# Kernel optimization log

Measured on AMD Instinct MI355X. Metric: run time of the kernel, lower is better.

## Reference

```python
import jax, jax.numpy as jnp
import numpy as np

N_ENTITY, N_REL, DIM, H = 500000, 32, 64, 2
N_ITEM, N_MEM, BATCH, HIST = 10000, 32, 4096, 50


def setup_inputs() -> dict:
    key = jax.random.key(0)
    ks = jax.random.split(key, 10)
    return {
        "entity_emb": jax.random.normal(ks[0], (N_ENTITY, DIM), jnp.float32) * 0.05,
        "relation_emb": jax.random.normal(ks[1], (N_REL, DIM), jnp.float32) * 0.05,
        "W_w": jax.random.normal(ks[2], (1, 3 * DIM), jnp.float32) * 0.05,
        "W_b": jnp.zeros((1,), jnp.float32),
        "item_ids": jax.random.randint(ks[3], (N_ITEM,), 0, N_ENTITY, jnp.int32),
        "heads": jax.random.randint(ks[4], (H, N_ITEM, N_MEM), 0, N_ENTITY, jnp.int32),
        "relations": jax.random.randint(ks[5], (H, N_ITEM, N_MEM), 0, N_REL, jnp.int32),
        "tails": jax.random.randint(ks[6], (H, N_ITEM, N_MEM), 0, N_ENTITY, jnp.int32),
        "records_idx": jax.random.randint(ks[7], (BATCH, HIST), 0, N_ITEM, jnp.int32),
        "items": jax.random.randint(ks[8], (BATCH,), 0, N_ENTITY, jnp.int32),
    }


def reference(entity_emb, relation_emb, W_w, W_b, item_ids, heads, relations, tails, records_idx, items):
    d = entity_emb.shape[1]
    # Split the Linear(3d->1) weight so we never materialize the [n_item,m,3d] concat.
    w_h, w_r, w_t = W_w[0, :d], W_w[0, d:2 * d], W_w[0, 2 * d:]
    # Hop-0 item embedding (base entity embedding of each candidate item).
    acc = entity_emb[item_ids]  # [n_item, d]
    for h in range(heads.shape[0]):
        te = entity_emb[tails[h]]  # [n_item, m, d]
        logits = (entity_emb[heads[h]] @ w_h
                  + relation_emb[relations[h]] @ w_r
                  + te @ w_t + W_b[0])  # [n_item, m]
        # Original: sigmoid then softmax over the memory axis.
        pi = jax.nn.softmax(jax.nn.sigmoid(logits), axis=1)[..., None]
        acc = acc + (pi * te).sum(axis=1)
    # User embedding = sum of (hop-enhanced) item embeddings over history records.
    user_emb = acc[records_idx].sum(axis=1)  # [B, d]
    pair_item = entity_emb[items]            # [B, d] (raw entity embedding)
    return jax.nn.sigmoid(jnp.sum(user_emb * pair_item, axis=-1))
```

## Files before the change

kernel.cpp:

```cpp
#include <hip/hip_runtime.h>
#include <math.h>

#define DIM      64
#define N_MEM    32
#define N_ENTITY 500000
#define N_REL    32
#define N_ITEM   10000
#define HOPS     2
#define BATCH    4096
#define HIST     50

typedef float4 f4;

__global__ __launch_bounds__(256) void ripple_rdot(
    const float* __restrict__ relation_emb,
    const float* __restrict__ W_w,
    float* __restrict__ rdot)
{
    const int wave = (blockIdx.x * blockDim.x + threadIdx.x) >> 6;
    const int lane = threadIdx.x & 63;
    const int g = lane >> 4;
    const int p = lane & 15;
    const int r = wave * 4 + g;
    if (r >= N_REL) return;
    const f4 wr = ((const f4*)W_w)[16 + p];
    const f4 r4 = ((const f4*)relation_emb)[(size_t)r * 16 + p];
    float vr = r4.x * wr.x + r4.y * wr.y + r4.z * wr.z + r4.w * wr.w;
    vr += __shfl_xor(vr, 1, 64);
    vr += __shfl_xor(vr, 2, 64);
    vr += __shfl_xor(vr, 4, 64);
    vr += __shfl_xor(vr, 8, 64);
    if (p == 0) rdot[r] = vr;
}

__global__ __launch_bounds__(256) void ripple_stage1(
    const float* __restrict__ W_w,
    const float* __restrict__ W_b,
    const int*   __restrict__ heads,
    const int*   __restrict__ relations,
    const int*   __restrict__ tails,
    const float* __restrict__ entity_emb,
    const float* __restrict__ rdot,
    float*       __restrict__ accp)
{
    const int wave = (blockIdx.x * blockDim.x + threadIdx.x) >> 6;
    const int lane = threadIdx.x & 63;
    if (wave >= HOPS * N_ITEM) return;
    const int h = wave < N_ITEM ? 0 : 1;
    const int i = wave - h * N_ITEM;
    const int g = lane >> 4;
    const int p = lane & 15;

    const f4* __restrict__ E4 = (const f4*)entity_emb;
    const f4* __restrict__ W4 = (const f4*)W_w;

    const f4 wh = W4[p];
    const f4 wt = W4[32 + p];
    const float bias = W_b[0];

    const int base = wave * N_MEM + g;

    int hi[8], ri[8], ti[8];
#pragma unroll
    for (int k = 0; k < 8; ++k) {
        hi[k] = heads[base + 4 * k];
        ri[k] = relations[base + 4 * k];
        ti[k] = tails[base + 4 * k];
    }

    f4 he[8], te[8];
#pragma unroll
    for (int k = 0; k < 8; ++k) he[k] = E4[(size_t)hi[k] * 16 + p];
#pragma unroll
    for (int k = 0; k < 8; ++k) te[k] = E4[(size_t)ti[k] * 16 + p];

    float lr[8];
#pragma unroll
    for (int k = 0; k < 8; ++k) lr[k] = rdot[ri[k]];

    float part[8];
#pragma unroll
    for (int k = 0; k < 8; ++k) {
        part[k] = he[k].x * wh.x + he[k].y * wh.y + he[k].z * wh.z + he[k].w * wh.w
                + te[k].x * wt.x + te[k].y * wt.y + te[k].z * wt.z + te[k].w * wt.w;
    }

    float e[8];
    float se = 0.f;
#pragma unroll
    for (int k = 0; k < 8; ++k) {
        float v = part[k];
        v += __shfl_xor(v, 1, 64);
        v += __shfl_xor(v, 2, 64);
        v += __shfl_xor(v, 4, 64);
        v += __shfl_xor(v, 8, 64);
        const float logit = v + lr[k] + bias;
        const float sig   = 1.f / (1.f + __expf(-logit));
        const float ex    = __expf(sig);
        e[k] = ex;
        se += ex;
    }
    se += __shfl_xor(se, 16, 64);
    se += __shfl_xor(se, 32, 64);
    const float inv = 1.f / se;

    f4 acc = {0.f, 0.f, 0.f, 0.f};
#pragma unroll
    for (int k = 0; k < 8; ++k) {
        const float w = e[k] * inv;
        acc.x += w * te[k].x;
        acc.y += w * te[k].y;
        acc.z += w * te[k].z;
        acc.w += w * te[k].w;
    }

    acc.x += __shfl_xor(acc.x, 16, 64);
    acc.x += __shfl_xor(acc.x, 32, 64);
    acc.y += __shfl_xor(acc.y, 16, 64);
    acc.y += __shfl_xor(acc.y, 32, 64);
    acc.z += __shfl_xor(acc.z, 16, 64);
    acc.z += __shfl_xor(acc.z, 32, 64);
    acc.w += __shfl_xor(acc.w, 16, 64);
    acc.w += __shfl_xor(acc.w, 32, 64);
    if (g == 0) ((f4*)accp)[((size_t)i * 2 + h) * 16 + p] = acc;
}

__global__ __launch_bounds__(256) void ripple_fold(
    const float* __restrict__ entity_emb,
    const int*   __restrict__ item_ids,
    const float* __restrict__ accp,
    float*       __restrict__ folded)
{
    const int t = blockIdx.x * blockDim.x + threadIdx.x;
    if (t >= N_ITEM * 16) return;
    const int i = t >> 4;
    const int p = t & 15;
    const f4* __restrict__ E4 = (const f4*)entity_emb;
    const f4* __restrict__ A4 = (const f4*)accp;
    const f4 a  = A4[(size_t)i * 32 + p];
    const f4 b  = A4[(size_t)i * 32 + 16 + p];
    const f4 it = E4[(size_t)item_ids[i] * 16 + p];
    f4 r;
    r.x = it.x + a.x + b.x;
    r.y = it.y + a.y + b.y;
    r.z = it.z + a.z + b.z;
    r.w = it.w + a.w + b.w;
    ((f4*)folded)[(size_t)i * 16 + p] = r;
}

__global__ __launch_bounds__(256) void ripple_stage2(
    const float* __restrict__ entity_emb,
    const int*   __restrict__ records_idx,
    const int*   __restrict__ items,
    const float* __restrict__ folded,
    float*       __restrict__ out)
{
    const int wave = (blockIdx.x * blockDim.x + threadIdx.x) >> 6;
    const int lane = threadIdx.x & 63;
    if (wave >= BATCH) return;
    const int b = wave;
    const int g = lane >> 4;
    const int p = lane & 15;

    const f4* __restrict__ A4 = (const f4*)folded;
    const f4* __restrict__ E4 = (const f4*)entity_emb;

    const int rb = b * HIST;
    int idx[13];
    float wgt[13];
#pragma unroll
    for (int k = 0; k < 13; ++k) {
        const int j  = 4 * k + g;
        const int jc = j < HIST ? j : (HIST - 1);
        wgt[k] = j < HIST ? 1.f : 0.f;
        idx[k] = records_idx[rb + jc];
    }

    f4 user = {0.f, 0.f, 0.f, 0.f};
#pragma unroll
    for (int k = 0; k < 13; ++k) {
        const f4 r = A4[(size_t)idx[k] * 16 + p];
        user.x += wgt[k] * r.x;
        user.y += wgt[k] * r.y;
        user.z += wgt[k] * r.z;
        user.w += wgt[k] * r.w;
    }
    user.x += __shfl_xor(user.x, 16, 64);
    user.x += __shfl_xor(user.x, 32, 64);
    user.y += __shfl_xor(user.y, 16, 64);
    user.y += __shfl_xor(user.y, 32, 64);
    user.z += __shfl_xor(user.z, 16, 64);
    user.z += __shfl_xor(user.z, 32, 64);
    user.w += __shfl_xor(user.w, 16, 64);
    user.w += __shfl_xor(user.w, 32, 64);

    const f4 pair = E4[(size_t)items[b] * 16 + p];
    float dot = user.x * pair.x + user.y * pair.y + user.z * pair.z + user.w * pair.w;
    dot += __shfl_xor(dot, 1, 64);
    dot += __shfl_xor(dot, 2, 64);
    dot += __shfl_xor(dot, 4, 64);
    dot += __shfl_xor(dot, 8, 64);
    if (lane == 0) out[b] = 1.f / (1.f + __expf(-dot));
}

extern "C" void kernel_launch(void* const* d_in, const int* in_sizes, int n_in,
                              void* d_out, int out_size, void* d_ws, size_t ws_size,
                              hipStream_t stream) {
    const float* entity_emb   = (const float*)d_in[0];
    const float* relation_emb = (const float*)d_in[1];
    const float* W_w          = (const float*)d_in[2];
    const float* W_b          = (const float*)d_in[3];
    const int*   item_ids     = (const int*)d_in[4];
    const int*   heads        = (const int*)d_in[5];
    const int*   relations    = (const int*)d_in[6];
    const int*   tails        = (const int*)d_in[7];
    const int*   records_idx  = (const int*)d_in[8];
    const int*   items        = (const int*)d_in[9];
    float* out = (float*)d_out;

    float* rdot   = (float*)d_ws;
    float* accp   = rdot + N_REL;
    float* folded = accp + (size_t)N_ITEM * HOPS * DIM;

    ripple_rdot<<<2, 256, 0, stream>>>(relation_emb, W_w, rdot);

    const int waves1  = HOPS * N_ITEM;
    const int blocks1 = (waves1 + 3) / 4;
    ripple_stage1<<<blocks1, 256, 0, stream>>>(W_w, W_b, heads, relations, tails,
                                               entity_emb, rdot, accp);

    const int blocksF = (N_ITEM * 16 + 255) / 256;
    ripple_fold<<<blocksF, 256, 0, stream>>>(entity_emb, item_ids, accp, folded);

    const int blocks2 = (BATCH + 3) / 4;
    ripple_stage2<<<blocks2, 256, 0, stream>>>(entity_emb, records_idx, items,
                                               folded, out);
}
```

Measured before the change: 228.3 us.

## Precompute per-entity head-weight dot products to replace head embedding gathers

Adds a pass that computes the dot product of every entity row with the head slice of the linear weight, alongside the relation dots. Stage1 then gathers a single float per head index instead of a full 64-float head embedding row and its dot product. This removes the random 256-byte head-row gathers from stage1. In exchange it streams the whole entity table once per call and writes a 500k-float workspace array, most of which is never used.

```diff
diff --git a/kernel.cpp b/kernel.cpp
--- a/kernel.cpp
+++ b/kernel.cpp
@@ -12,25 +12,39 @@
 
 typedef float4 f4;
 
-__global__ __launch_bounds__(256) void ripple_rdot(
+__global__ __launch_bounds__(256) void ripple_dots(
+    const float* __restrict__ entity_emb,
     const float* __restrict__ relation_emb,
     const float* __restrict__ W_w,
+    float* __restrict__ hdot,
     float* __restrict__ rdot)
 {
     const int wave = (blockIdx.x * blockDim.x + threadIdx.x) >> 6;
     const int lane = threadIdx.x & 63;
     const int g = lane >> 4;
     const int p = lane & 15;
-    const int r = wave * 4 + g;
-    if (r >= N_REL) return;
-    const f4 wr = ((const f4*)W_w)[16 + p];
-    const f4 r4 = ((const f4*)relation_emb)[(size_t)r * 16 + p];
-    float vr = r4.x * wr.x + r4.y * wr.y + r4.z * wr.z + r4.w * wr.w;
-    vr += __shfl_xor(vr, 1, 64);
-    vr += __shfl_xor(vr, 2, 64);
-    vr += __shfl_xor(vr, 4, 64);
-    vr += __shfl_xor(vr, 8, 64);
-    if (p == 0) rdot[r] = vr;
+    const int row = wave * 4 + g;
+    if (row >= N_ENTITY + N_REL) return;
+
+    const f4* __restrict__ W4 = (const f4*)W_w;
+    float v;
+    if (row < N_ENTITY) {
+        const f4 w = W4[p];
+        const f4 e = ((const f4*)entity_emb)[(size_t)row * 16 + p];
+        v = e.x * w.x + e.y * w.y + e.z * w.z + e.w * w.w;
+    } else {
+        const f4 w = W4[16 + p];
+        const f4 e = ((const f4*)relation_emb)[(size_t)(row - N_ENTITY) * 16 + p];
+        v = e.x * w.x + e.y * w.y + e.z * w.z + e.w * w.w;
+    }
+    v += __shfl_xor(v, 1, 64);
+    v += __shfl_xor(v, 2, 64);
+    v += __shfl_xor(v, 4, 64);
+    v += __shfl_xor(v, 8, 64);
+    if (p == 0) {
+        if (row < N_ENTITY) hdot[row] = v;
+        else                rdot[row - N_ENTITY] = v;
+    }
 }
 
 __global__ __launch_bounds__(256) void ripple_stage1(
@@ -40,6 +54,7 @@
     const int*   __restrict__ relations,
     const int*   __restrict__ tails,
     const float* __restrict__ entity_emb,
+    const float* __restrict__ hdot,
     const float* __restrict__ rdot,
     float*       __restrict__ accp)
 {
@@ -54,7 +69,6 @@
     const f4* __restrict__ E4 = (const f4*)entity_emb;
     const f4* __restrict__ W4 = (const f4*)W_w;
 
-    const f4 wh = W4[p];
     const f4 wt = W4[32 + p];
     const float bias = W_b[0];
 
@@ -68,21 +82,20 @@
         ti[k] = tails[base + 4 * k];
     }
 
-    f4 he[8], te[8];
-#pragma unroll
-    for (int k = 0; k < 8; ++k) he[k] = E4[(size_t)hi[k] * 16 + p];
+    f4 te[8];
 #pragma unroll
     for (int k = 0; k < 8; ++k) te[k] = E4[(size_t)ti[k] * 16 + p];
 
-    float lr[8];
+    float lh[8], lr[8];
+#pragma unroll
+    for (int k = 0; k < 8; ++k) lh[k] = hdot[hi[k]];
 #pragma unroll
     for (int k = 0; k < 8; ++k) lr[k] = rdot[ri[k]];
 
     float part[8];
 #pragma unroll
     for (int k = 0; k < 8; ++k) {
-        part[k] = he[k].x * wh.x + he[k].y * wh.y + he[k].z * wh.z + he[k].w * wh.w
-                + te[k].x * wt.x + te[k].y * wt.y + te[k].z * wt.z + te[k].w * wt.w;
+        part[k] = te[k].x * wt.x + te[k].y * wt.y + te[k].z * wt.z + te[k].w * wt.w;
     }
 
     float e[8];
@@ -94,7 +107,7 @@
         v += __shfl_xor(v, 2, 64);
         v += __shfl_xor(v, 4, 64);
         v += __shfl_xor(v, 8, 64);
-        const float logit = v + lr[k] + bias;
+        const float logit = v + lh[k] + lr[k] + bias;
         const float sig   = 1.f / (1.f + __expf(-logit));
         const float ex    = __expf(sig);
         e[k] = ex;
@@ -219,15 +232,18 @@
     float* out = (float*)d_out;
 
     float* rdot   = (float*)d_ws;
-    float* accp   = rdot + N_REL;
+    float* hdot   = rdot + N_REL;
+    float* accp   = hdot + N_ENTITY;
     float* folded = accp + (size_t)N_ITEM * HOPS * DIM;
 
-    ripple_rdot<<<2, 256, 0, stream>>>(relation_emb, W_w, rdot);
+    const int rowsD   = N_ENTITY + N_REL;
+    const int blocksD = (rowsD + 15) / 16;
+    ripple_dots<<<blocksD, 256, 0, stream>>>(entity_emb, relation_emb, W_w, hdot, rdot);
 
     const int waves1  = HOPS * N_ITEM;
     const int blocks1 = (waves1 + 3) / 4;
     ripple_stage1<<<blocks1, 256, 0, stream>>>(W_w, W_b, heads, relations, tails,
-                                               entity_emb, rdot, accp);
+                                               entity_emb, hdot, rdot, accp);
 
     const int blocksF = (N_ITEM * 16 + 255) / 256;
     ripple_fold<<<blocksF, 256, 0, stream>>>(entity_emb, item_ids, accp, folded);
```

Measured after the change: 235.2 us. +3.0%, slower.

## Fuse both hops and fold into one stage1 wave; shuffle-broadcast indices

Applied to the files above, without the earlier changes.

Stage1 now assigns one wave per item that processes both hops and adds the base item embedding, which removes the separate fold kernel and the accp intermediate buffer. Head, relation and tail indices, plus the relation dot, are loaded once per lane with coalesced reads and broadcast with __shfl, replacing the strided per-group loads. Stage2 likewise loads the history indices once per lane and broadcasts them. In exchange the grid has half as many waves with more serial work per wave and higher register pressure, which reduces the memory-latency parallelism available for the random gathers.

```diff
diff --git a/kernel.cpp b/kernel.cpp
--- a/kernel.cpp
+++ b/kernel.cpp
@@ -41,111 +41,99 @@
     const int*   __restrict__ tails,
     const float* __restrict__ entity_emb,
     const float* __restrict__ rdot,
-    float*       __restrict__ accp)
+    const int*   __restrict__ item_ids,
+    float*       __restrict__ folded)
 {
     const int wave = (blockIdx.x * blockDim.x + threadIdx.x) >> 6;
     const int lane = threadIdx.x & 63;
-    if (wave >= HOPS * N_ITEM) return;
-    const int h = wave < N_ITEM ? 0 : 1;
-    const int i = wave - h * N_ITEM;
+    if (wave >= N_ITEM) return;
+    const int i = wave;
     const int g = lane >> 4;
     const int p = lane & 15;
 
     const f4* __restrict__ E4 = (const f4*)entity_emb;
     const f4* __restrict__ W4 = (const f4*)W_w;
-
     const f4 wh = W4[p];
     const f4 wt = W4[32 + p];
     const float bias = W_b[0];
 
-    const int base = wave * N_MEM + g;
-
-    int hi[8], ri[8], ti[8];
-#pragma unroll
-    for (int k = 0; k < 8; ++k) {
-        hi[k] = heads[base + 4 * k];
-        ri[k] = relations[base + 4 * k];
-        ti[k] = tails[base + 4 * k];
+    const int m    = lane & 31;
+    const int hsel = lane >> 5;
+    const size_t idxoff = (size_t)hsel * ((size_t)N_ITEM * N_MEM)
+                        + (size_t)i * N_MEM + m;
+    const int   hidx = heads[idxoff];
+    const int   ridx = relations[idxoff];
+    const int   tidx = tails[idxoff];
+    const float lrl  = rdot[ridx];
+
+    const f4 item = E4[(size_t)item_ids[i] * 16 + p];
+
+    f4 accs[2];
+#pragma unroll
+    for (int h = 0; h < 2; ++h) {
+        int hi[8], ti[8]; float lrv[8];
+#pragma unroll
+        for (int k = 0; k < 8; ++k) {
+            const int src = h * 32 + 4 * k + g;
+            hi[k]  = __shfl(hidx, src, 64);
+            ti[k]  = __shfl(tidx, src, 64);
+            lrv[k] = __shfl(lrl,  src, 64);
+        }
+
+        f4 he[8], te[8];
+#pragma unroll
+        for (int k = 0; k < 8; ++k) he[k] = E4[(size_t)hi[k] * 16 + p];
+#pragma unroll
+        for (int k = 0; k < 8; ++k) te[k] = E4[(size_t)ti[k] * 16 + p];
+
+        float e[8];
+        float se = 0.f;
+#pragma unroll
+        for (int k = 0; k < 8; ++k) {
+            float v = he[k].x * wh.x + he[k].y * wh.y + he[k].z * wh.z + he[k].w * wh.w
+                    + te[k].x * wt.x + te[k].y * wt.y + te[k].z * wt.z + te[k].w * wt.w;
+            v += __shfl_xor(v, 1, 64);
+            v += __shfl_xor(v, 2, 64);
+            v += __shfl_xor(v, 4, 64);
+            v += __shfl_xor(v, 8, 64);
+            const float logit = v + lrv[k] + bias;
+            const float sig   = 1.f / (1.f + __expf(-logit));
+            const float ex    = __expf(sig);
+            e[k] = ex;
+            se += ex;
+        }
+        se += __shfl_xor(se, 16, 64);
+        se += __shfl_xor(se, 32, 64);
+        const float inv = 1.f / se;
+
+        f4 acc = {0.f, 0.f, 0.f, 0.f};
+#pragma unroll
+        for (int k = 0; k < 8; ++k) {
+            const float w = e[k] * inv;
+            acc.x += w * te[k].x;
+            acc.y += w * te[k].y;
+            acc.z += w * te[k].z;
+            acc.w += w * te[k].w;
+        }
+        acc.x += __shfl_xor(acc.x, 16, 64);
+        acc.x += __shfl_xor(acc.x, 32, 64);
+        acc.y += __shfl_xor(acc.y, 16, 64);
+        acc.y += __shfl_xor(acc.y, 32, 64);
+        acc.z += __shfl_xor(acc.z, 16, 64);
+        acc.z += __shfl_xor(acc.z, 32, 64);
+        acc.w += __shfl_xor(acc.w, 16, 64);
+        acc.w += __shfl_xor(acc.w, 32, 64);
+        accs[h] = acc;
     }
 
-    f4 he[8], te[8];
-#pragma unroll
-    for (int k = 0; k < 8; ++k) he[k] = E4[(size_t)hi[k] * 16 + p];
-#pragma unroll
-    for (int k = 0; k < 8; ++k) te[k] = E4[(size_t)ti[k] * 16 + p];
-
-    float lr[8];
-#pragma unroll
-    for (int k = 0; k < 8; ++k) lr[k] = rdot[ri[k]];
-
-    float part[8];
-#pragma unroll
-    for (int k = 0; k < 8; ++k) {
-        part[k] = he[k].x * wh.x + he[k].y * wh.y + he[k].z * wh.z + he[k].w * wh.w
-                + te[k].x * wt.x + te[k].y * wt.y + te[k].z * wt.z + te[k].w * wt.w;
+    if (g == 0) {
+        f4 r;
+        r.x = item.x + accs[0].x + accs[1].x;
+        r.y = item.y + accs[0].y + accs[1].y;
+        r.z = item.z + accs[0].z + accs[1].z;
+        r.w = item.w + accs[0].w + accs[1].w;
+        ((f4*)folded)[(size_t)i * 16 + p] = r;
     }
-
-    float e[8];
-    float se = 0.f;
-#pragma unroll
-    for (int k = 0; k < 8; ++k) {
-        float v = part[k];
-        v += __shfl_xor(v, 1, 64);
-        v += __shfl_xor(v, 2, 64);
-        v += __shfl_xor(v, 4, 64);
-        v += __shfl_xor(v, 8, 64);
-        const float logit = v + lr[k] + bias;
-        const float sig   = 1.f / (1.f + __expf(-logit));
-        const float ex    = __expf(sig);
-        e[k] = ex;
-        se += ex;
-    }
-    se += __shfl_xor(se, 16, 64);
-    se += __shfl_xor(se, 32, 64);
-    const float inv = 1.f / se;
-
-    f4 acc = {0.f, 0.f, 0.f, 0.f};
-#pragma unroll
-    for (int k = 0; k < 8; ++k) {
-        const float w = e[k] * inv;
-        acc.x += w * te[k].x;
-        acc.y += w * te[k].y;
-        acc.z += w * te[k].z;
-        acc.w += w * te[k].w;
-    }
-
-    acc.x += __shfl_xor(acc.x, 16, 64);
-    acc.x += __shfl_xor(acc.x, 32, 64);
-    acc.y += __shfl_xor(acc.y, 16, 64);
-    acc.y += __shfl_xor(acc.y, 32, 64);
-    acc.z += __shfl_xor(acc.z, 16, 64);
-    acc.z += __shfl_xor(acc.z, 32, 64);
-    acc.w += __shfl_xor(acc.w, 16, 64);
-    acc.w += __shfl_xor(acc.w, 32, 64);
-    if (g == 0) ((f4*)accp)[((size_t)i * 2 + h) * 16 + p] = acc;
-}
-
-__global__ __launch_bounds__(256) void ripple_fold(
-    const float* __restrict__ entity_emb,
-    const int*   __restrict__ item_ids,
-    const float* __restrict__ accp,
-    float*       __restrict__ folded)
-{
-    const int t = blockIdx.x * blockDim.x + threadIdx.x;
-    if (t >= N_ITEM * 16) return;
-    const int i = t >> 4;
-    const int p = t & 15;
-    const f4* __restrict__ E4 = (const f4*)entity_emb;
-    const f4* __restrict__ A4 = (const f4*)accp;
-    const f4 a  = A4[(size_t)i * 32 + p];
-    const f4 b  = A4[(size_t)i * 32 + 16 + p];
-    const f4 it = E4[(size_t)item_ids[i] * 16 + p];
-    f4 r;
-    r.x = it.x + a.x + b.x;
-    r.y = it.y + a.y + b.y;
-    r.z = it.z + a.z + b.z;
-    r.w = it.w + a.w + b.w;
-    ((f4*)folded)[(size_t)i * 16 + p] = r;
 }
 
 __global__ __launch_bounds__(256) void ripple_stage2(
@@ -166,24 +154,21 @@
     const f4* __restrict__ E4 = (const f4*)entity_emb;
 
     const int rb = b * HIST;
-    int idx[13];
-    float wgt[13];
+    const int lc = lane < HIST ? lane : (HIST - 1);
+    const int idxl = records_idx[rb + lc];
+
+    f4 user = {0.f, 0.f, 0.f, 0.f};
 #pragma unroll
     for (int k = 0; k < 13; ++k) {
-        const int j  = 4 * k + g;
-        const int jc = j < HIST ? j : (HIST - 1);
-        wgt[k] = j < HIST ? 1.f : 0.f;
-        idx[k] = records_idx[rb + jc];
-    }
-
-    f4 user = {0.f, 0.f, 0.f, 0.f};
-#pragma unroll
-    for (int k = 0; k < 13; ++k) {
-        const f4 r = A4[(size_t)idx[k] * 16 + p];
-        user.x += wgt[k] * r.x;
-        user.y += wgt[k] * r.y;
-        user.z += wgt[k] * r.z;
-        user.w += wgt[k] * r.w;
+        const int   j  = 4 * k + g;
+        const int   js = j < HIST ? j : 0;
+        const float w  = j < HIST ? 1.f : 0.f;
+        const int  idx = __shfl(idxl, js, 64);
+        const f4 r = A4[(size_t)idx * 16 + p];
+        user.x += w * r.x;
+        user.y += w * r.y;
+        user.z += w * r.z;
+        user.w += w * r.w;
     }
     user.x += __shfl_xor(user.x, 16, 64);
     user.x += __shfl_xor(user.x, 32, 64);
@@ -219,18 +204,13 @@
     float* out = (float*)d_out;
 
     float* rdot   = (float*)d_ws;
-    float* accp   = rdot + N_REL;
-    float* folded = accp + (size_t)N_ITEM * HOPS * DIM;
+    float* folded = rdot + N_REL;
 
     ripple_rdot<<<2, 256, 0, stream>>>(relation_emb, W_w, rdot);
 
-    const int waves1  = HOPS * N_ITEM;
-    const int blocks1 = (waves1 + 3) / 4;
+    const int blocks1 = (N_ITEM + 3) / 4;
     ripple_stage1<<<blocks1, 256, 0, stream>>>(W_w, W_b, heads, relations, tails,
-                                               entity_emb, rdot, accp);
-
-    const int blocksF = (N_ITEM * 16 + 255) / 256;
-    ripple_fold<<<blocksF, 256, 0, stream>>>(entity_emb, item_ids, accp, folded);
+                                               entity_emb, rdot, item_ids, folded);
 
     const int blocks2 = (BATCH + 3) / 4;
     ripple_stage2<<<blocks2, 256, 0, stream>>>(entity_emb, records_idx, items,
```

Measured after the change: 225.5 us. Within noise of the previous version (-1.2%).
